# Optimization experiments

Hardware: AMD Instinct MI355X
Metric: run time of the kernel (lower is better)

## Reference

```python
import jax, jax.numpy as jnp
import numpy as np

N_NODES = 50000
N_EDGES = 800000
N_FEAT, N_HID, N_LATENT = 512, 256, 128


def spmm(rows, cols, vals, dense):
    # out[r] += vals[e] * dense[cols[e]]  -- COO SpMM via segment_sum
    gathered = dense[cols] * vals[:, None]          # [E, d]
    return jax.ops.segment_sum(gathered, rows, num_segments=N_NODES)


def setup_inputs() -> dict:
    key = jax.random.key(0)
    ks = jax.random.split(key, 8)
    x = jax.random.normal(ks[0], (N_NODES, N_FEAT), dtype=jnp.float32)
    edge_rows = jax.random.randint(ks[1], (N_EDGES,), 0, N_NODES, dtype=jnp.int32)
    edge_cols = jax.random.randint(ks[2], (N_EDGES,), 0, N_NODES, dtype=jnp.int32)
    edge_vals = jax.random.uniform(ks[3], (N_EDGES,), dtype=jnp.float32)
    # Glorot-style init like the torch GraphConvolution
    W1 = jax.random.normal(ks[4], (N_FEAT, N_HID), dtype=jnp.float32) / np.sqrt(N_FEAT)
    b1 = jnp.zeros((N_HID,), dtype=jnp.float32)
    W2 = jax.random.normal(ks[5], (N_HID, N_LATENT), dtype=jnp.float32) / np.sqrt(N_HID)
    b2 = jnp.zeros((N_LATENT,), dtype=jnp.float32)
    return {"x": x, "edge_rows": edge_rows, "edge_cols": edge_cols,
            "edge_vals": edge_vals, "W1": W1, "b1": b1, "W2": W2, "b2": b2}


def reference(x, edge_rows, edge_cols, edge_vals, W1, b1, W2, b2):
    # layer 1: relu(adj @ (x @ W1) + b1)
    h = spmm(edge_rows, edge_cols, edge_vals, x @ W1) + b1
    h = jax.nn.relu(h)
    # layer 2: relu(adj @ (h @ W2) + b2)
    z = spmm(edge_rows, edge_cols, edge_vals, h @ W2) + b2
    return jax.nn.relu(z)
```

## Files before the change

### kernel.cpp

```cpp
#include <hip/hip_runtime.h>
#include <hip/hip_bf16.h>


typedef __attribute__((ext_vector_type(8))) short bf16x8;
typedef __attribute__((ext_vector_type(4))) float f32x4;

#define NN 50000
#define NE 800000
#define NF 512
#define NH 256
#define NL 128
#define NB ((NN + 255) / 256)

static __device__ __forceinline__ unsigned short f2bf(float f) {
  union { float f; unsigned int u; } v; v.f = f;
  unsigned int r = v.u + 0x7fffu + ((v.u >> 16) & 1u);
  return (unsigned short)(r >> 16);
}
static __device__ __forceinline__ float bf2f(unsigned short u) {
  union { unsigned int u; float f; } v; v.u = (unsigned int)u << 16;
  return v.f;
}

static __device__ __forceinline__ unsigned int pkbf(float lo, float hi) {
  unsigned int r;
  asm("v_cvt_pk_bf16_f32 %0, %1, %2" : "=v"(r) : "v"(lo), "v"(hi));
  return r;
}
static __device__ __forceinline__ uint4 pk8(float4 a, float4 b) {
  uint4 o;
  o.x = pkbf(a.x, a.y); o.y = pkbf(a.z, a.w);
  o.z = pkbf(b.x, b.y); o.w = pkbf(b.z, b.w);
  return o;
}

static __device__ __forceinline__ void gll16(const void* g, void* l) {
  __builtin_amdgcn_global_load_lds(
      (const __attribute__((address_space(1))) void*)g,
      (__attribute__((address_space(3))) void*)l, 16, 0, 0);
}

extern "C" __global__ void k_hist(const int* __restrict__ rows, int* __restrict__ counts, int n) {
  int i = blockIdx.x * 256 + threadIdx.x;
  if (i < n) atomicAdd(&counts[rows[i]], 1);
}

extern "C" __global__ __launch_bounds__(256) void k_blocksum(
    const int* __restrict__ counts, int* __restrict__ bsum, int n) {
  __shared__ int s[256];
  int t = threadIdx.x;
  int i = blockIdx.x * 256 + t;
  s[t] = (i < n) ? counts[i] : 0;
  __syncthreads();
  for (int off = 128; off > 0; off >>= 1) {
    if (t < off) s[t] += s[t + off];
    __syncthreads();
  }
  if (t == 0) bsum[blockIdx.x] = s[0];
}

extern "C" __global__ __launch_bounds__(256) void k_scansums(
    const int* __restrict__ bsum, int* __restrict__ bpre, int* __restrict__ rp, int nb, int n) {
  __shared__ int s[256];
  int t = threadIdx.x;
  int v = (t < nb) ? bsum[t] : 0;
  s[t] = v;
  __syncthreads();
  for (int off = 1; off < 256; off <<= 1) {
    int u = (t >= off) ? s[t - off] : 0;
    __syncthreads();
    s[t] += u;
    __syncthreads();
  }
  if (t < nb) bpre[t] = s[t] - v;
  if (t == 255) rp[n] = s[255];
}

extern "C" __global__ __launch_bounds__(256) void k_scanfin(
    const int* __restrict__ counts, const int* __restrict__ bpre,
    int* __restrict__ rp, int* __restrict__ cur, int n) {
  __shared__ int s[256];
  int t = threadIdx.x;
  int i = blockIdx.x * 256 + t;
  int c = (i < n) ? counts[i] : 0;
  s[t] = c;
  __syncthreads();
  for (int off = 1; off < 256; off <<= 1) {
    int u = (t >= off) ? s[t - off] : 0;
    __syncthreads();
    s[t] += u;
    __syncthreads();
  }
  if (i < n) {
    int e = bpre[blockIdx.x] + s[t] - c;
    rp[i] = e;
    cur[i] = e;
  }
}

extern "C" __global__ void k_scatter(const int* __restrict__ rows, const int* __restrict__ cols,
    const float* __restrict__ vals, int* __restrict__ cur, int2* __restrict__ ep, int n) {
  int i = blockIdx.x * 256 + threadIdx.x;
  if (i < n) {
    int p = atomicAdd(&cur[rows[i]], 1);
    int2 e; e.x = cols[i]; e.y = __float_as_int(vals[i]);
    ep[p] = e;
  }
}

extern "C" __global__ void k_transcast(const float* __restrict__ w, unsigned short* __restrict__ wt,
                                       int K, int N) {
  int k = blockIdx.x; int n = threadIdx.x;
  wt[(size_t)n * K + k] = f2bf(w[(size_t)k * N + n]);
}

extern "C" __global__ __launch_bounds__(256, 2) void k_gemm1(
    const float* __restrict__ A, const unsigned short* __restrict__ BT,
    unsigned short* __restrict__ C) {
  __shared__ __align__(16) unsigned short sB[2][32 * 512];
  int tid = threadIdx.x;
  int lane = tid & 63, wid = tid >> 6;
  int l15 = lane & 15, lq = lane >> 4;
  int bm = blockIdx.x * 64;

  auto issueB = [&](int q, int b) {
#pragma unroll
    for (int j = 0; j < 8; ++j) {
      int u = tid + 256 * j;
      int c = u >> 6, cu = u & 63;
      int g = cu ^ (c & 7);
      gll16(BT + (size_t)(q * 32 + c) * NF + g * 8, &sB[b][u * 8]);
    }
  };

  int arow = bm + wid * 16 + l15; if (arow >= NN) arow = NN - 1;
  const float* ap = A + (size_t)arow * NF + lq * 8;

  issueB(0, 0);
  float4 apf[4][2];
#pragma unroll
  for (int p = 0; p < 4; ++p) {
    apf[p][0] = *(const float4*)(ap + p * 32);
    apf[p][1] = *(const float4*)(ap + p * 32 + 4);
  }
  __syncthreads();
  issueB(1, 1);

  bf16x8 abf[16];
  f32x4 acc[16];
#pragma unroll
  for (int i = 0; i < 16; ++i) acc[i] = (f32x4){0.f, 0.f, 0.f, 0.f};

#pragma unroll
  for (int p = 0; p < 16; ++p) {
    bf16x8 bfr[2];
#pragma unroll
    for (int nt = 0; nt < 2; ++nt) {
      int c = nt * 16 + l15;
      int u = (p * 4 + lq) ^ (c & 7);
      bfr[nt] = *(const bf16x8*)(&sB[0][c * 512 + u * 8]);
    }
    union { uint4 u; bf16x8 v; } cv;
    cv.u = pk8(apf[p & 3][0], apf[p & 3][1]);
    abf[p] = cv.v;
    if (p < 12) {
      apf[p & 3][0] = *(const float4*)(ap + (p + 4) * 32);
      apf[p & 3][1] = *(const float4*)(ap + (p + 4) * 32 + 4);
    }
#pragma unroll
    for (int nt = 0; nt < 2; ++nt)
      acc[nt] = __builtin_amdgcn_mfma_f32_16x16x32_bf16(abf[p], bfr[nt], acc[nt], 0, 0, 0);
  }
  __syncthreads();

#pragma unroll
  for (int q = 1; q < 8; ++q) {
    if (q < 7) issueB(q + 1, (q + 1) & 1);
#pragma unroll
    for (int p = 0; p < 16; ++p) {
      bf16x8 bfr[2];
#pragma unroll
      for (int nt = 0; nt < 2; ++nt) {
        int c = nt * 16 + l15;
        int u = (p * 4 + lq) ^ (c & 7);
        bfr[nt] = *(const bf16x8*)(&sB[q & 1][c * 512 + u * 8]);
      }
#pragma unroll
      for (int nt = 0; nt < 2; ++nt)
        acc[q * 2 + nt] = __builtin_amdgcn_mfma_f32_16x16x32_bf16(abf[p], bfr[nt], acc[q * 2 + nt], 0, 0, 0);
    }
    if (q < 7) __syncthreads();
  }

#pragma unroll
  for (int t = 0; t < 16; ++t) {
#pragma unroll
    for (int r = 0; r < 4; ++r) {
      int gr = bm + wid * 16 + lq * 4 + r;
      if (gr < NN) {
        int gc = t * 16 + l15;
        C[(size_t)gr * NH + gc] = f2bf(acc[t][r]);
      }
    }
  }
}

extern "C" __global__ __launch_bounds__(256, 2) void k_gemm2(
    const unsigned short* __restrict__ Ah, const unsigned short* __restrict__ BT,
    unsigned short* __restrict__ C) {
  __shared__ __align__(16) unsigned short sB[128 * 256];
  int tid = threadIdx.x;
  int lane = tid & 63, wid = tid >> 6;
  int l15 = lane & 15, lq = lane >> 4;
  int bm = blockIdx.x * 64;

#pragma unroll
  for (int j = 0; j < 16; ++j) {
    int u = tid + 256 * j;
    int row = u >> 5, cu = u & 31;
    int g = cu ^ (row & 7);
    gll16(BT + (size_t)row * NH + g * 8, &sB[u * 8]);
  }

  int arow = bm + wid * 16 + l15; if (arow >= NN) arow = NN - 1;
  const unsigned short* ap = Ah + (size_t)arow * NH + lq * 8;

  bf16x8 apf[4];
#pragma unroll
  for (int p = 0; p < 4; ++p) apf[p] = *(const bf16x8*)(ap + p * 32);

  __syncthreads();

  f32x4 acc[8];
#pragma unroll
  for (int i = 0; i < 8; ++i) acc[i] = (f32x4){0.f, 0.f, 0.f, 0.f};

#pragma unroll
  for (int p = 0; p < 8; ++p) {
    bf16x8 bfr[8];
#pragma unroll
    for (int nt = 0; nt < 8; ++nt) {
      int c = nt * 16 + l15;
      int u = (p * 4 + lq) ^ (c & 7);
      bfr[nt] = *(const bf16x8*)(&sB[c * 256 + u * 8]);
    }
    bf16x8 af = apf[p & 3];
    if (p < 4) apf[p & 3] = *(const bf16x8*)(ap + (p + 4) * 32);
#pragma unroll
    for (int nt = 0; nt < 8; ++nt)
      acc[nt] = __builtin_amdgcn_mfma_f32_16x16x32_bf16(af, bfr[nt], acc[nt], 0, 0, 0);
  }

#pragma unroll
  for (int nt = 0; nt < 8; ++nt) {
#pragma unroll
    for (int r = 0; r < 4; ++r) {
      int gr = bm + wid * 16 + lq * 4 + r;
      if (gr < NN) {
        int gc = nt * 16 + l15;
        C[(size_t)gr * NL + gc] = f2bf(acc[nt][r]);
      }
    }
  }
}

extern "C" __global__ __launch_bounds__(256) void k_spmm256(
    const int* __restrict__ rp, const int2* __restrict__ ep,
    const unsigned short* __restrict__ src, const float* __restrict__ bias,
    ushort4* __restrict__ out) {
  int row = blockIdx.x * 4 + (threadIdx.x >> 6);
  int lane = threadIdx.x & 63;
  if (row >= NN) return;
  int e0 = __builtin_amdgcn_readfirstlane(rp[row]);
  int e1 = __builtin_amdgcn_readfirstlane(rp[row + 1]);
  const ushort4* srcv = (const ushort4*)src;
  float4 acc = {0.f, 0.f, 0.f, 0.f};
  int e = e0;
  for (; e + 8 <= e1; e += 8) {
    int2 p[8]; ushort4 g[8];
#pragma unroll
    for (int j = 0; j < 8; ++j) p[j] = ep[e + j];
#pragma unroll
    for (int j = 0; j < 8; ++j) g[j] = srcv[(size_t)p[j].x * (NH / 4) + lane];
#pragma unroll
    for (int j = 0; j < 8; ++j) {
      float v = __int_as_float(p[j].y);
      acc.x = fmaf(v, bf2f(g[j].x), acc.x); acc.y = fmaf(v, bf2f(g[j].y), acc.y);
      acc.z = fmaf(v, bf2f(g[j].z), acc.z); acc.w = fmaf(v, bf2f(g[j].w), acc.w);
    }
  }
  for (; e + 4 <= e1; e += 4) {
    int2 p[4]; ushort4 g[4];
#pragma unroll
    for (int j = 0; j < 4; ++j) p[j] = ep[e + j];
#pragma unroll
    for (int j = 0; j < 4; ++j) g[j] = srcv[(size_t)p[j].x * (NH / 4) + lane];
#pragma unroll
    for (int j = 0; j < 4; ++j) {
      float v = __int_as_float(p[j].y);
      acc.x = fmaf(v, bf2f(g[j].x), acc.x); acc.y = fmaf(v, bf2f(g[j].y), acc.y);
      acc.z = fmaf(v, bf2f(g[j].z), acc.z); acc.w = fmaf(v, bf2f(g[j].w), acc.w);
    }
  }
  for (; e < e1; ++e) {
    int2 p = ep[e];
    float v = __int_as_float(p.y);
    ushort4 g = srcv[(size_t)p.x * (NH / 4) + lane];
    acc.x = fmaf(v, bf2f(g.x), acc.x); acc.y = fmaf(v, bf2f(g.y), acc.y);
    acc.z = fmaf(v, bf2f(g.z), acc.z); acc.w = fmaf(v, bf2f(g.w), acc.w);
  }
  float4 b = ((const float4*)bias)[lane];
  ushort4 o;
  o.x = f2bf(fmaxf(acc.x + b.x, 0.f));
  o.y = f2bf(fmaxf(acc.y + b.y, 0.f));
  o.z = f2bf(fmaxf(acc.z + b.z, 0.f));
  o.w = f2bf(fmaxf(acc.w + b.w, 0.f));
  out[(size_t)row * (NH / 4) + lane] = o;
}

extern "C" __global__ __launch_bounds__(256) void k_spmm128(
    const int* __restrict__ rp, const int2* __restrict__ ep,
    const unsigned short* __restrict__ src, const float* __restrict__ bias,
    float2* __restrict__ out) {
  int row = blockIdx.x * 4 + (threadIdx.x >> 6);
  int lane = threadIdx.x & 63;
  if (row >= NN) return;
  int e0 = __builtin_amdgcn_readfirstlane(rp[row]);
  int e1 = __builtin_amdgcn_readfirstlane(rp[row + 1]);
  const ushort2* srcv = (const ushort2*)src;
  float2 acc = {0.f, 0.f};
  int e = e0;
  for (; e + 8 <= e1; e += 8) {
    int2 p[8]; ushort2 g[8];
#pragma unroll
    for (int j = 0; j < 8; ++j) p[j] = ep[e + j];
#pragma unroll
    for (int j = 0; j < 8; ++j) g[j] = srcv[(size_t)p[j].x * (NL / 2) + lane];
#pragma unroll
    for (int j = 0; j < 8; ++j) {
      float v = __int_as_float(p[j].y);
      acc.x = fmaf(v, bf2f(g[j].x), acc.x); acc.y = fmaf(v, bf2f(g[j].y), acc.y);
    }
  }
  for (; e + 4 <= e1; e += 4) {
    int2 p[4]; ushort2 g[4];
#pragma unroll
    for (int j = 0; j < 4; ++j) p[j] = ep[e + j];
#pragma unroll
    for (int j = 0; j < 4; ++j) g[j] = srcv[(size_t)p[j].x * (NL / 2) + lane];
#pragma unroll
    for (int j = 0; j < 4; ++j) {
      float v = __int_as_float(p[j].y);
      acc.x = fmaf(v, bf2f(g[j].x), acc.x); acc.y = fmaf(v, bf2f(g[j].y), acc.y);
    }
  }
  for (; e < e1; ++e) {
    int2 p = ep[e];
    float v = __int_as_float(p.y);
    ushort2 g = srcv[(size_t)p.x * (NL / 2) + lane];
    acc.x = fmaf(v, bf2f(g.x), acc.x); acc.y = fmaf(v, bf2f(g.y), acc.y);
  }
  float2 b = ((const float2*)bias)[lane];
  float2 o;
  o.x = fmaxf(acc.x + b.x, 0.f);
  o.y = fmaxf(acc.y + b.y, 0.f);
  out[(size_t)row * (NL / 2) + lane] = o;
}

extern "C" void kernel_launch(void* const* d_in, const int* in_sizes, int n_in,
                              void* d_out, int out_size, void* d_ws, size_t ws_size,
                              hipStream_t stream) {
  const float* x   = (const float*)d_in[0];
  const int* erow  = (const int*)d_in[1];
  const int* ecol  = (const int*)d_in[2];
  const float* ev  = (const float*)d_in[3];
  const float* W1  = (const float*)d_in[4];
  const float* b1  = (const float*)d_in[5];
  const float* W2  = (const float*)d_in[6];
  const float* b2  = (const float*)d_in[7];

  char* ws = (char*)d_ws;
  unsigned short* xwb = (unsigned short*)(ws + 0);
  unsigned short* hbf = (unsigned short*)(ws + 25600000);
  unsigned short* hwb = (unsigned short*)(ws + 51200000);
  unsigned short* w1t = (unsigned short*)(ws + 64000000);
  unsigned short* w2t = (unsigned short*)(ws + 64262144);
  int* rp    = (int*)(ws + 64327680);
  int* cur   = (int*)(ws + 64528384);
  int* cnt   = (int*)(ws + 64729088);
  int* bsum  = (int*)(ws + 64929792);
  int* bpre  = (int*)(ws + 64930816);
  int2* ep   = (int2*)(ws + 64931840);

  hipMemsetAsync(cnt, 0, NN * sizeof(int), stream);
  k_hist<<<NE / 256, 256, 0, stream>>>(erow, cnt, NE);
  k_blocksum<<<NB, 256, 0, stream>>>(cnt, bsum, NN);
  k_scansums<<<1, 256, 0, stream>>>(bsum, bpre, rp, NB, NN);
  k_scanfin<<<NB, 256, 0, stream>>>(cnt, bpre, rp, cur, NN);
  k_scatter<<<NE / 256, 256, 0, stream>>>(erow, ecol, ev, cur, ep, NE);

  k_transcast<<<NF, NH, 0, stream>>>(W1, w1t, NF, NH);
  k_gemm1<<<(NN + 63) / 64, 256, 0, stream>>>(x, w1t, xwb);
  k_spmm256<<<NN / 4, 256, 0, stream>>>(rp, ep, xwb, b1, (ushort4*)hbf);

  k_transcast<<<NH, NL, 0, stream>>>(W2, w2t, NH, NL);
  k_gemm2<<<(NN + 63) / 64, 256, 0, stream>>>(hbf, w2t, hwb);
  k_spmm128<<<NN / 4, 256, 0, stream>>>(rp, ep, hwb, b2, (float2*)d_out);
}
```

Measured before the change: 382.2 us.

## Fuse layer-1 SpMM with second GEMM and merge weight transposes

The layer-1 SpMM kernel now aggregates 16 rows per block into shared memory, then multiplies that tile by W2 with MFMA in the same kernel. This drops the separate gemm2 kernel and the write and re-read of the hidden activation buffer. The two weight transpose-casts are also merged into one launch. In exchange, each block reads W2 fragments straight from global memory rather than staging them in LDS. Blocks are also coarser, at 4 rows per wave run one after another, which may reduce latency hiding on the gather.

```diff
diff --git a/kernel.cpp b/kernel.cpp
--- a/kernel.cpp
+++ b/kernel.cpp
@@ -108,10 +108,15 @@
   }
 }
 
-extern "C" __global__ void k_transcast(const float* __restrict__ w, unsigned short* __restrict__ wt,
-                                       int K, int N) {
-  int k = blockIdx.x; int n = threadIdx.x;
-  wt[(size_t)n * K + k] = f2bf(w[(size_t)k * N + n]);
+extern "C" __global__ void k_transcast2(const float* __restrict__ W1, unsigned short* __restrict__ w1t,
+                                        const float* __restrict__ W2, unsigned short* __restrict__ w2t) {
+  int b = blockIdx.x, n = threadIdx.x;
+  if (b < NF) {
+    w1t[(size_t)n * NF + b] = f2bf(W1[(size_t)b * NH + n]);
+  } else {
+    int k = b - NF;
+    if (n < NL) w2t[(size_t)n * NH + k] = f2bf(W2[(size_t)k * NL + n]);
+  }
 }
 
 extern "C" __global__ __launch_bounds__(256, 2) void k_gemm1(
@@ -205,117 +210,92 @@
   }
 }
 
-extern "C" __global__ __launch_bounds__(256, 2) void k_gemm2(
-    const unsigned short* __restrict__ Ah, const unsigned short* __restrict__ BT,
-    unsigned short* __restrict__ C) {
-  __shared__ __align__(16) unsigned short sB[128 * 256];
-  int tid = threadIdx.x;
-  int lane = tid & 63, wid = tid >> 6;
-  int l15 = lane & 15, lq = lane >> 4;
-  int bm = blockIdx.x * 64;
-
-#pragma unroll
-  for (int j = 0; j < 16; ++j) {
-    int u = tid + 256 * j;
-    int row = u >> 5, cu = u & 31;
-    int g = cu ^ (row & 7);
-    gll16(BT + (size_t)row * NH + g * 8, &sB[u * 8]);
-  }
-
-  int arow = bm + wid * 16 + l15; if (arow >= NN) arow = NN - 1;
-  const unsigned short* ap = Ah + (size_t)arow * NH + lq * 8;
-
-  bf16x8 apf[4];
-#pragma unroll
-  for (int p = 0; p < 4; ++p) apf[p] = *(const bf16x8*)(ap + p * 32);
-
-  __syncthreads();
-
-  f32x4 acc[8];
-#pragma unroll
-  for (int i = 0; i < 8; ++i) acc[i] = (f32x4){0.f, 0.f, 0.f, 0.f};
-
-#pragma unroll
-  for (int p = 0; p < 8; ++p) {
-    bf16x8 bfr[8];
-#pragma unroll
-    for (int nt = 0; nt < 8; ++nt) {
-      int c = nt * 16 + l15;
-      int u = (p * 4 + lq) ^ (c & 7);
-      bfr[nt] = *(const bf16x8*)(&sB[c * 256 + u * 8]);
-    }
-    bf16x8 af = apf[p & 3];
-    if (p < 4) apf[p & 3] = *(const bf16x8*)(ap + (p + 4) * 32);
-#pragma unroll
-    for (int nt = 0; nt < 8; ++nt)
-      acc[nt] = __builtin_amdgcn_mfma_f32_16x16x32_bf16(af, bfr[nt], acc[nt], 0, 0, 0);
-  }
-
-#pragma unroll
-  for (int nt = 0; nt < 8; ++nt) {
-#pragma unroll
-    for (int r = 0; r < 4; ++r) {
-      int gr = bm + wid * 16 + lq * 4 + r;
-      if (gr < NN) {
-        int gc = nt * 16 + l15;
-        C[(size_t)gr * NL + gc] = f2bf(acc[nt][r]);
-      }
-    }
-  }
-}
-
-extern "C" __global__ __launch_bounds__(256) void k_spmm256(
+extern "C" __global__ __launch_bounds__(256) void k_spmm256g2(
     const int* __restrict__ rp, const int2* __restrict__ ep,
     const unsigned short* __restrict__ src, const float* __restrict__ bias,
-    ushort4* __restrict__ out) {
-  int row = blockIdx.x * 4 + (threadIdx.x >> 6);
-  int lane = threadIdx.x & 63;
-  if (row >= NN) return;
-  int e0 = __builtin_amdgcn_readfirstlane(rp[row]);
-  int e1 = __builtin_amdgcn_readfirstlane(rp[row + 1]);
+    const unsigned short* __restrict__ w2t, unsigned short* __restrict__ hwb) {
+  __shared__ __align__(16) unsigned short sh[16][264];
+  int base = blockIdx.x * 16;
+  int lane = threadIdx.x & 63, w = threadIdx.x >> 6;
   const ushort4* srcv = (const ushort4*)src;
-  float4 acc = {0.f, 0.f, 0.f, 0.f};
-  int e = e0;
-  for (; e + 8 <= e1; e += 8) {
-    int2 p[8]; ushort4 g[8];
-#pragma unroll
-    for (int j = 0; j < 8; ++j) p[j] = ep[e + j];
-#pragma unroll
-    for (int j = 0; j < 8; ++j) g[j] = srcv[(size_t)p[j].x * (NH / 4) + lane];
-#pragma unroll
-    for (int j = 0; j < 8; ++j) {
-      float v = __int_as_float(p[j].y);
-      acc.x = fmaf(v, bf2f(g[j].x), acc.x); acc.y = fmaf(v, bf2f(g[j].y), acc.y);
-      acc.z = fmaf(v, bf2f(g[j].z), acc.z); acc.w = fmaf(v, bf2f(g[j].w), acc.w);
-    }
-  }
-  for (; e + 4 <= e1; e += 4) {
-    int2 p[4]; ushort4 g[4];
-#pragma unroll
-    for (int j = 0; j < 4; ++j) p[j] = ep[e + j];
-#pragma unroll
-    for (int j = 0; j < 4; ++j) g[j] = srcv[(size_t)p[j].x * (NH / 4) + lane];
-#pragma unroll
-    for (int j = 0; j < 4; ++j) {
-      float v = __int_as_float(p[j].y);
-      acc.x = fmaf(v, bf2f(g[j].x), acc.x); acc.y = fmaf(v, bf2f(g[j].y), acc.y);
-      acc.z = fmaf(v, bf2f(g[j].z), acc.z); acc.w = fmaf(v, bf2f(g[j].w), acc.w);
-    }
-  }
-  for (; e < e1; ++e) {
-    int2 p = ep[e];
-    float v = __int_as_float(p.y);
-    ushort4 g = srcv[(size_t)p.x * (NH / 4) + lane];
-    acc.x = fmaf(v, bf2f(g.x), acc.x); acc.y = fmaf(v, bf2f(g.y), acc.y);
-    acc.z = fmaf(v, bf2f(g.z), acc.z); acc.w = fmaf(v, bf2f(g.w), acc.w);
-  }
   float4 b = ((const float4*)bias)[lane];
-  ushort4 o;
-  o.x = f2bf(fmaxf(acc.x + b.x, 0.f));
-  o.y = f2bf(fmaxf(acc.y + b.y, 0.f));
-  o.z = f2bf(fmaxf(acc.z + b.z, 0.f));
-  o.w = f2bf(fmaxf(acc.w + b.w, 0.f));
-  out[(size_t)row * (NH / 4) + lane] = o;
+
+#pragma unroll
+  for (int i = 0; i < 4; ++i) {
+    int rl = w + i * 4;
+    int row = base + rl;
+    int e0 = __builtin_amdgcn_readfirstlane(rp[row]);
+    int e1 = __builtin_amdgcn_readfirstlane(rp[row + 1]);
+    float4 acc = {0.f, 0.f, 0.f, 0.f};
+    int e = e0;
+    for (; e + 8 <= e1; e += 8) {
+      int2 p[8]; ushort4 g[8];
+#pragma unroll
+      for (int j = 0; j < 8; ++j) p[j] = ep[e + j];
+#pragma unroll
+      for (int j = 0; j < 8; ++j) g[j] = srcv[(size_t)p[j].x * (NH / 4) + lane];
+#pragma unroll
+      for (int j = 0; j < 8; ++j) {
+        float v = __int_as_float(p[j].y);
+        acc.x = fmaf(v, bf2f(g[j].x), acc.x); acc.y = fmaf(v, bf2f(g[j].y), acc.y);
+        acc.z = fmaf(v, bf2f(g[j].z), acc.z); acc.w = fmaf(v, bf2f(g[j].w), acc.w);
+      }
+    }
+    for (; e + 4 <= e1; e += 4) {
+      int2 p[4]; ushort4 g[4];
+#pragma unroll
+      for (int j = 0; j < 4; ++j) p[j] = ep[e + j];
+#pragma unroll
+      for (int j = 0; j < 4; ++j) g[j] = srcv[(size_t)p[j].x * (NH / 4) + lane];
+#pragma unroll
+      for (int j = 0; j < 4; ++j) {
+        float v = __int_as_float(p[j].y);
+        acc.x = fmaf(v, bf2f(g[j].x), acc.x); acc.y = fmaf(v, bf2f(g[j].y), acc.y);
+        acc.z = fmaf(v, bf2f(g[j].z), acc.z); acc.w = fmaf(v, bf2f(g[j].w), acc.w);
+      }
+    }
+    for (; e < e1; ++e) {
+      int2 p = ep[e];
+      float v = __int_as_float(p.y);
+      ushort4 g = srcv[(size_t)p.x * (NH / 4) + lane];
+      acc.x = fmaf(v, bf2f(g.x), acc.x); acc.y = fmaf(v, bf2f(g.y), acc.y);
+      acc.z = fmaf(v, bf2f(g.z), acc.z); acc.w = fmaf(v, bf2f(g.w), acc.w);
+    }
+    ushort4 o;
+    o.x = f2bf(fmaxf(acc.x + b.x, 0.f));
+    o.y = f2bf(fmaxf(acc.y + b.y, 0.f));
+    o.z = f2bf(fmaxf(acc.z + b.z, 0.f));
+    o.w = f2bf(fmaxf(acc.w + b.w, 0.f));
+    *(ushort4*)(&sh[rl][lane * 4]) = o;
+  }
+  __syncthreads();
+
+  int l15 = lane & 15, lq = lane >> 4;
+  f32x4 acc2[2];
+  acc2[0] = (f32x4){0.f, 0.f, 0.f, 0.f};
+  acc2[1] = (f32x4){0.f, 0.f, 0.f, 0.f};
+  const unsigned short* bp[2];
+#pragma unroll
+  for (int t = 0; t < 2; ++t)
+    bp[t] = w2t + (size_t)(w * 32 + t * 16 + l15) * NH + lq * 8;
+#pragma unroll
+  for (int ks = 0; ks < 8; ++ks) {
+    bf16x8 af = *(const bf16x8*)(&sh[l15][ks * 32 + lq * 8]);
+#pragma unroll
+    for (int t = 0; t < 2; ++t) {
+      bf16x8 bfr = *(const bf16x8*)(bp[t] + ks * 32);
+      acc2[t] = __builtin_amdgcn_mfma_f32_16x16x32_bf16(af, bfr, acc2[t], 0, 0, 0);
+    }
+  }
+#pragma unroll
+  for (int t = 0; t < 2; ++t) {
+#pragma unroll
+    for (int r = 0; r < 4; ++r) {
+      int gr = base + lq * 4 + r;
+      int gc = w * 32 + t * 16 + l15;
+      hwb[(size_t)gr * NL + gc] = f2bf(acc2[t][r]);
+    }
+  }
 }
 
 extern "C" __global__ __launch_bounds__(256) void k_spmm128(
@@ -381,7 +361,6 @@
 
   char* ws = (char*)d_ws;
   unsigned short* xwb = (unsigned short*)(ws + 0);
-  unsigned short* hbf = (unsigned short*)(ws + 25600000);
   unsigned short* hwb = (unsigned short*)(ws + 51200000);
   unsigned short* w1t = (unsigned short*)(ws + 64000000);
   unsigned short* w2t = (unsigned short*)(ws + 64262144);
@@ -399,11 +378,11 @@
   k_scanfin<<<NB, 256, 0, stream>>>(cnt, bpre, rp, cur, NN);
   k_scatter<<<NE / 256, 256, 0, stream>>>(erow, ecol, ev, cur, ep, NE);
 
-  k_transcast<<<NF, NH, 0, stream>>>(W1, w1t, NF, NH);
+  k_transcast2<<<NF + NH, NH, 0, stream>>>(W1, w1t, W2, w2t);
+
   k_gemm1<<<(NN + 63) / 64, 256, 0, stream>>>(x, w1t, xwb);
-  k_spmm256<<<NN / 4, 256, 0, stream>>>(rp, ep, xwb, b1, (ushort4*)hbf);
-
-  k_transcast<<<NH, NL, 0, stream>>>(W2, w2t, NH, NL);
-  k_gemm2<<<(NN + 63) / 64, 256, 0, stream>>>(hbf, w2t, hwb);
+
+  k_spmm256g2<<<NN / 16, 256, 0, stream>>>(rp, ep, xwb, b1, w2t, hwb);
+
   k_spmm128<<<NN / 4, 256, 0, stream>>>(rp, ep, hwb, b2, (float2*)d_out);
 }
```

Measured after the change: 380.6 us. No clear change (-0.4%).

## Split SpMM feature columns into chunks across blocks and merge weight transposes

Applied to the files above, without the earlier changes.

Both SpMM kernels now launch eight blocks per row group. Each block handles one column chunk, and the lanes of a wave are split between columns and interleaved edges, with the partial sums combined by cross-lane shuffles. The goal is more parallelism and latency hiding per row, at the cost of narrow 2-byte gathers that coalesce poorly, and edge metadata is re-read by every chunk. The two weight transpose-cast kernels are also merged into one launch.

```diff
diff --git a/kernel.cpp b/kernel.cpp
--- a/kernel.cpp
+++ b/kernel.cpp
@@ -108,10 +108,15 @@
   }
 }
 
-extern "C" __global__ void k_transcast(const float* __restrict__ w, unsigned short* __restrict__ wt,
-                                       int K, int N) {
-  int k = blockIdx.x; int n = threadIdx.x;
-  wt[(size_t)n * K + k] = f2bf(w[(size_t)k * N + n]);
+extern "C" __global__ void k_transcast2(const float* __restrict__ W1, unsigned short* __restrict__ w1t,
+                                        const float* __restrict__ W2, unsigned short* __restrict__ w2t) {
+  int b = blockIdx.x, n = threadIdx.x;
+  if (b < NF) {
+    w1t[(size_t)n * NF + b] = f2bf(W1[(size_t)b * NH + n]);
+  } else {
+    int k = b - NF;
+    if (n < NL) w2t[(size_t)n * NH + k] = f2bf(W2[(size_t)k * NL + n]);
+  }
 }
 
 extern "C" __global__ __launch_bounds__(256, 2) void k_gemm1(
@@ -264,107 +269,85 @@
   }
 }
 
-extern "C" __global__ __launch_bounds__(256) void k_spmm256(
+extern "C" __global__ __launch_bounds__(256) void k_spmm256c(
     const int* __restrict__ rp, const int2* __restrict__ ep,
     const unsigned short* __restrict__ src, const float* __restrict__ bias,
-    ushort4* __restrict__ out) {
-  int row = blockIdx.x * 4 + (threadIdx.x >> 6);
+    unsigned short* __restrict__ out) {
+  int bid = blockIdx.x;
+  int chunk = bid & 7;
+  int row = (bid >> 3) * 4 + (threadIdx.x >> 6);
   int lane = threadIdx.x & 63;
-  if (row >= NN) return;
+  int col = lane & 31, eoff = lane >> 5;
+  int cbase = chunk * 32;
   int e0 = __builtin_amdgcn_readfirstlane(rp[row]);
   int e1 = __builtin_amdgcn_readfirstlane(rp[row + 1]);
-  const ushort4* srcv = (const ushort4*)src;
-  float4 acc = {0.f, 0.f, 0.f, 0.f};
+  const unsigned short* sc = src + cbase + col;
+  float acc = 0.f;
   int e = e0;
-  for (; e + 8 <= e1; e += 8) {
-    int2 p[8]; ushort4 g[8];
-#pragma unroll
-    for (int j = 0; j < 8; ++j) p[j] = ep[e + j];
-#pragma unroll
-    for (int j = 0; j < 8; ++j) g[j] = srcv[(size_t)p[j].x * (NH / 4) + lane];
-#pragma unroll
-    for (int j = 0; j < 8; ++j) {
-      float v = __int_as_float(p[j].y);
-      acc.x = fmaf(v, bf2f(g[j].x), acc.x); acc.y = fmaf(v, bf2f(g[j].y), acc.y);
-      acc.z = fmaf(v, bf2f(g[j].z), acc.z); acc.w = fmaf(v, bf2f(g[j].w), acc.w);
-    }
-  }
-  for (; e + 4 <= e1; e += 4) {
-    int2 p[4]; ushort4 g[4];
-#pragma unroll
-    for (int j = 0; j < 4; ++j) p[j] = ep[e + j];
-#pragma unroll
-    for (int j = 0; j < 4; ++j) g[j] = srcv[(size_t)p[j].x * (NH / 4) + lane];
-#pragma unroll
-    for (int j = 0; j < 4; ++j) {
-      float v = __int_as_float(p[j].y);
-      acc.x = fmaf(v, bf2f(g[j].x), acc.x); acc.y = fmaf(v, bf2f(g[j].y), acc.y);
-      acc.z = fmaf(v, bf2f(g[j].z), acc.z); acc.w = fmaf(v, bf2f(g[j].w), acc.w);
-    }
-  }
-  for (; e < e1; ++e) {
+  for (; e + 16 <= e1; e += 16) {
+    int2 p[8]; unsigned short g[8];
+#pragma unroll
+    for (int j = 0; j < 8; ++j) p[j] = ep[e + j * 2 + eoff];
+#pragma unroll
+    for (int j = 0; j < 8; ++j) g[j] = sc[(size_t)p[j].x * NH];
+#pragma unroll
+    for (int j = 0; j < 8; ++j)
+      acc = fmaf(__int_as_float(p[j].y), bf2f(g[j]), acc);
+  }
+  for (; e + 2 <= e1; e += 2) {
+    int2 p = ep[e + eoff];
+    acc = fmaf(__int_as_float(p.y), bf2f(sc[(size_t)p.x * NH]), acc);
+  }
+  if (e < e1 && eoff == 0) {
     int2 p = ep[e];
-    float v = __int_as_float(p.y);
-    ushort4 g = srcv[(size_t)p.x * (NH / 4) + lane];
-    acc.x = fmaf(v, bf2f(g.x), acc.x); acc.y = fmaf(v, bf2f(g.y), acc.y);
-    acc.z = fmaf(v, bf2f(g.z), acc.z); acc.w = fmaf(v, bf2f(g.w), acc.w);
-  }
-  float4 b = ((const float4*)bias)[lane];
-  ushort4 o;
-  o.x = f2bf(fmaxf(acc.x + b.x, 0.f));
-  o.y = f2bf(fmaxf(acc.y + b.y, 0.f));
-  o.z = f2bf(fmaxf(acc.z + b.z, 0.f));
-  o.w = f2bf(fmaxf(acc.w + b.w, 0.f));
-  out[(size_t)row * (NH / 4) + lane] = o;
-}
-
-extern "C" __global__ __launch_bounds__(256) void k_spmm128(
+    acc = fmaf(__int_as_float(p.y), bf2f(sc[(size_t)p.x * NH]), acc);
+  }
+  acc += __shfl_xor(acc, 32);
+  if (eoff == 0) {
+    float v = fmaxf(acc + bias[cbase + col], 0.f);
+    out[(size_t)row * NH + cbase + col] = f2bf(v);
+  }
+}
+
+extern "C" __global__ __launch_bounds__(256) void k_spmm128c(
     const int* __restrict__ rp, const int2* __restrict__ ep,
     const unsigned short* __restrict__ src, const float* __restrict__ bias,
-    float2* __restrict__ out) {
-  int row = blockIdx.x * 4 + (threadIdx.x >> 6);
+    float* __restrict__ out) {
+  int bid = blockIdx.x;
+  int chunk = bid & 7;
+  int row = (bid >> 3) * 4 + (threadIdx.x >> 6);
   int lane = threadIdx.x & 63;
-  if (row >= NN) return;
+  int col = lane & 15, eoff = lane >> 4;
+  int cbase = chunk * 16;
   int e0 = __builtin_amdgcn_readfirstlane(rp[row]);
   int e1 = __builtin_amdgcn_readfirstlane(rp[row + 1]);
-  const ushort2* srcv = (const ushort2*)src;
-  float2 acc = {0.f, 0.f};
+  const unsigned short* sc = src + cbase + col;
+  float acc = 0.f;
   int e = e0;
-  for (; e + 8 <= e1; e += 8) {
-    int2 p[8]; ushort2 g[8];
-#pragma unroll
-    for (int j = 0; j < 8; ++j) p[j] = ep[e + j];
-#pragma unroll
-    for (int j = 0; j < 8; ++j) g[j] = srcv[(size_t)p[j].x * (NL / 2) + lane];
-#pragma unroll
-    for (int j = 0; j < 8; ++j) {
-      float v = __int_as_float(p[j].y);
-      acc.x = fmaf(v, bf2f(g[j].x), acc.x); acc.y = fmaf(v, bf2f(g[j].y), acc.y);
-    }
+  for (; e + 16 <= e1; e += 16) {
+    int2 p[4]; unsigned short g[4];
+#pragma unroll
+    for (int j = 0; j < 4; ++j) p[j] = ep[e + j * 4 + eoff];
+#pragma unroll
+    for (int j = 0; j < 4; ++j) g[j] = sc[(size_t)p[j].x * NL];
+#pragma unroll
+    for (int j = 0; j < 4; ++j)
+      acc = fmaf(__int_as_float(p[j].y), bf2f(g[j]), acc);
   }
   for (; e + 4 <= e1; e += 4) {
-    int2 p[4]; ushort2 g[4];
-#pragma unroll
-    for (int j = 0; j < 4; ++j) p[j] = ep[e + j];
-#pragma unroll
-    for (int j = 0; j < 4; ++j) g[j] = srcv[(size_t)p[j].x * (NL / 2) + lane];
-#pragma unroll
-    for (int j = 0; j < 4; ++j) {
-      float v = __int_as_float(p[j].y);
-      acc.x = fmaf(v, bf2f(g[j].x), acc.x); acc.y = fmaf(v, bf2f(g[j].y), acc.y);
-    }
-  }
-  for (; e < e1; ++e) {
-    int2 p = ep[e];
-    float v = __int_as_float(p.y);
-    ushort2 g = srcv[(size_t)p.x * (NL / 2) + lane];
-    acc.x = fmaf(v, bf2f(g.x), acc.x); acc.y = fmaf(v, bf2f(g.y), acc.y);
-  }
-  float2 b = ((const float2*)bias)[lane];
-  float2 o;
-  o.x = fmaxf(acc.x + b.x, 0.f);
-  o.y = fmaxf(acc.y + b.y, 0.f);
-  out[(size_t)row * (NL / 2) + lane] = o;
+    int2 p = ep[e + eoff];
+    acc = fmaf(__int_as_float(p.y), bf2f(sc[(size_t)p.x * NL]), acc);
+  }
+  int r = e1 - e;
+  if (eoff < r) {
+    int2 p = ep[e + eoff];
+    acc = fmaf(__int_as_float(p.y), bf2f(sc[(size_t)p.x * NL]), acc);
+  }
+  acc += __shfl_xor(acc, 16);
+  acc += __shfl_xor(acc, 32);
+  if (eoff == 0) {
+    out[(size_t)row * NL + cbase + col] = fmaxf(acc + bias[cbase + col], 0.f);
+  }
 }
 
 extern "C" void kernel_launch(void* const* d_in, const int* in_sizes, int n_in,
@@ -399,11 +382,11 @@
   k_scanfin<<<NB, 256, 0, stream>>>(cnt, bpre, rp, cur, NN);
   k_scatter<<<NE / 256, 256, 0, stream>>>(erow, ecol, ev, cur, ep, NE);
 
-  k_transcast<<<NF, NH, 0, stream>>>(W1, w1t, NF, NH);
+  k_transcast2<<<NF + NH, NH, 0, stream>>>(W1, w1t, W2, w2t);
+
   k_gemm1<<<(NN + 63) / 64, 256, 0, stream>>>(x, w1t, xwb);
-  k_spmm256<<<NN / 4, 256, 0, stream>>>(rp, ep, xwb, b1, (ushort4*)hbf);
-
-  k_transcast<<<NH, NL, 0, stream>>>(W2, w2t, NH, NL);
+  k_spmm256c<<<8 * (NN / 4), 256, 0, stream>>>(rp, ep, xwb, b1, hbf);
+
   k_gemm2<<<(NN + 63) / 64, 256, 0, stream>>>(hbf, w2t, hwb);
-  k_spmm128<<<NN / 4, 256, 0, stream>>>(rp, ep, hwb, b2, (float2*)d_out);
-}
+  k_spmm128c<<<8 * (NN / 4), 256, 0, stream>>>(rp, ep, hwb, b2, (float*)d_out);
+}
```

Result: slower. 674.6 us (+76.5%).
